# Kernel optimization log

Hardware: AMD Instinct MI355X
Metric: run time of the kernel (lower is better)

Reference implementation:

```python
import jax, jax.numpy as jnp
import numpy as np

DMODEL = 1024
N_EXPERTS = 16
EXPERT_SIZE = 256
K = 4


def setup_inputs() -> dict:
    key = jax.random.key(0)
    k1, k2, k3, k4 = jax.random.split(key, 4)
    std_sel = 1.0 / np.sqrt(DMODEL)
    std_val = 1.0 / np.sqrt(N_EXPERTS * EXPERT_SIZE)
    return {
        "x": jax.random.normal(k1, (4, 2048, DMODEL), dtype=jnp.float32),
        "expert_sel": jax.random.normal(k2, (N_EXPERTS, DMODEL), dtype=jnp.float32) * std_sel,
        "keys": jax.random.normal(k3, (N_EXPERTS, DMODEL, EXPERT_SIZE), dtype=jnp.float32) * std_sel,
        "values": jax.random.normal(k4, (N_EXPERTS, EXPERT_SIZE, DMODEL), dtype=jnp.float32) * std_val,
        "route_scale": jnp.ones((1,), dtype=jnp.float32),
    }


def reference(x, expert_sel, keys, values, route_scale):
    # Routing: sigmoid gating, top-k selection (eval mode: no dropout/bias balancing)
    sel_logits = jnp.einsum("btd,ed->bte", x, expert_sel)  # [B,T,E]
    sel_probs = jax.nn.sigmoid(sel_logits)
    _, sel_index = jax.lax.top_k(sel_probs, K)  # [B,T,K]
    sel_val = jnp.take_along_axis(sel_probs, sel_index, axis=-1)  # [B,T,K]
    sel_val = sel_val / jnp.clip(sel_val.sum(-1, keepdims=True), 1e-9)
    sel_val = sel_val * route_scale  # route_scale shape [1] broadcasts
    # Dense all-expert FFN (as in original), then gather top-k and combine
    scores_all = jax.nn.relu(jnp.einsum("btd,edh->bteh", x, keys))  # [B,T,E,H]
    values_all = jnp.einsum("bteh,ehv->btev", scores_all, values)   # [B,T,E,V]
    sel_idx_exp = sel_index[..., None]  # [B,T,K,1]
    selected = jnp.take_along_axis(values_all, sel_idx_exp, axis=2)  # [B,T,K,V]
    out = (selected * sel_val[..., None]).sum(axis=2)  # [B,T,V]
    return out
```

## Files before the change

### kernel.cpp

```cpp
#include <hip/hip_runtime.h>
#include <math.h>


constexpr int NTOK = 8192;
constexpr int DM   = 1024;
constexpr int NE   = 16;
constexpr int EH   = 256;
constexpr int TK   = 4;
constexpr int CAP  = 8192;
constexpr int TM   = 64;

typedef __attribute__((ext_vector_type(8))) short short8;
typedef __attribute__((ext_vector_type(4))) float f32x4;

#define MFMA16(a, b, c) __builtin_amdgcn_mfma_f32_16x16x32_bf16(a, b, c, 0, 0, 0)

__device__ __forceinline__ void gload_lds16(const void* g, void* l) {
    __builtin_amdgcn_global_load_lds(
        (const __attribute__((address_space(1))) void*)g,
        (__attribute__((address_space(3))) void*)l, 16, 0, 0);
}

__device__ __forceinline__ unsigned short f2bf(float f) {
    union { float f; unsigned int u; } x; x.f = f;
    unsigned int r = x.u + 0x7fffu + ((x.u >> 16) & 1u);
    return (unsigned short)(r >> 16);
}
__device__ __forceinline__ float bf2f(unsigned short b) {
    union { unsigned int u; float f; } x; x.u = ((unsigned int)b) << 16;
    return x.f;
}

__global__ __launch_bounds__(256) void route_conv_kernel(
    const float* __restrict__ x, const float* __restrict__ esel,
    const float* __restrict__ rscale,
    unsigned short* __restrict__ xb,
    int4* __restrict__ sel4, float* __restrict__ wtk)
{
    __shared__ float Es[NE * DM];
    int tid = threadIdx.x;

    {
        const float4* src = (const float4*)esel;
        float4* dst = (float4*)Es;
        #pragma unroll
        for (int j = 0; j < 16; ++j) dst[tid + j * 256] = src[tid + j * 256];
    }
    __syncthreads();

    int t    = blockIdx.x * 8 + (tid >> 5);
    int l32  = tid & 31;

    float acc[NE];
    #pragma unroll
    for (int e = 0; e < NE; ++e) acc[e] = 0.f;

    const float4* x4 = (const float4*)(x + (size_t)t * DM);
    const float4* E4 = (const float4*)Es;
    #pragma unroll
    for (int i4 = 0; i4 < 8; ++i4) {
        int d4 = i4 * 32 + l32;
        float4 xv = x4[d4];
        ushort4 cb = { f2bf(xv.x), f2bf(xv.y), f2bf(xv.z), f2bf(xv.w) };
        *(ushort4*)(xb + (size_t)t * DM + d4 * 4) = cb;
        #pragma unroll
        for (int e = 0; e < NE; ++e) {
            float4 wv = E4[e * 256 + d4];
            acc[e] = fmaf(xv.x, wv.x, acc[e]);
            acc[e] = fmaf(xv.y, wv.y, acc[e]);
            acc[e] = fmaf(xv.z, wv.z, acc[e]);
            acc[e] = fmaf(xv.w, wv.w, acc[e]);
        }
    }

    #pragma unroll
    for (int off = 16; off; off >>= 1)
        #pragma unroll
        for (int e = 0; e < NE; ++e)
            acc[e] += __shfl_xor(acc[e], off, 32);

    if (l32 == 0) {
        float p[NE];
        #pragma unroll
        for (int e = 0; e < NE; ++e) p[e] = 1.0f / (1.0f + expf(-acc[e]));

        int   sel_e[TK];
        float sel_p[TK];
        float sum = 0.f;
        #pragma unroll
        for (int k = 0; k < TK; ++k) {
            float best = -INFINITY; int be = NE;
            #pragma unroll
            for (int e = 0; e < NE; ++e) {
                bool take = p[e] > best;
                best = take ? p[e] : best;
                be   = take ? e    : be;
            }
            sel_e[k] = be; sel_p[k] = best; sum += best;
            #pragma unroll
            for (int e = 0; e < NE; ++e) p[e] = (e == be) ? -INFINITY : p[e];
        }

        float wsc = rscale[0] / fmaxf(sum, 1e-9f);
        int4 s = { sel_e[0], sel_e[1], sel_e[2], sel_e[3] };
        sel4[t] = s;
        float4 wv = { sel_p[0] * wsc, sel_p[1] * wsc,
                      sel_p[2] * wsc, sel_p[3] * wsc };
        *(float4*)(wtk + t * TK) = wv;
    }
}

__global__ __launch_bounds__(1024) void compact_kernel(
    const int4* __restrict__ sel4, int* __restrict__ counts,
    int* __restrict__ lpk)
{
    __shared__ int wsum[16];
    int e    = blockIdx.x;
    int tid  = threadIdx.x;
    int w    = tid >> 6;
    int lane = tid & 63;

    int base = 0;
    for (int c = 0; c < NTOK; c += 1024) {
        int t = c + tid;
        int4 s = sel4[t];
        int k = -1;
        if      (s.x == e) k = 0;
        else if (s.y == e) k = 1;
        else if (s.z == e) k = 2;
        else if (s.w == e) k = 3;
        unsigned long long m = __ballot(k >= 0);
        int rank = __popcll(m & ((1ull << lane) - 1ull));
        if (lane == 63) wsum[w] = __popcll(m);
        __syncthreads();
        int prefix = 0, total = 0;
        #pragma unroll
        for (int i = 0; i < 16; ++i) {
            int v = wsum[i];
            prefix += (i < w) ? v : 0;
            total  += v;
        }
        if (k >= 0) lpk[e * CAP + base + prefix + rank] = t * TK + k;
        base += total;
        __syncthreads();
    }
    if (tid == 0) counts[e] = base;
}

__global__ __launch_bounds__(256) void trans_kernel(
    const float* __restrict__ in, unsigned short* __restrict__ outp, int R, int C)
{
    __shared__ float T[32][33];
    int e = blockIdx.z;
    int r0 = blockIdx.y * 32, c0 = blockIdx.x * 32;
    int ri = threadIdx.x >> 3, cq = threadIdx.x & 7;
    float4 v = *(const float4*)(in + ((size_t)e * R + r0 + ri) * C + c0 + cq * 4);
    T[ri][cq * 4 + 0] = v.x; T[ri][cq * 4 + 1] = v.y;
    T[ri][cq * 4 + 2] = v.z; T[ri][cq * 4 + 3] = v.w;
    __syncthreads();
    int ci = threadIdx.x >> 3, rq = threadIdx.x & 7;
    ushort4 o = { f2bf(T[rq * 4 + 0][ci]), f2bf(T[rq * 4 + 1][ci]),
                  f2bf(T[rq * 4 + 2][ci]), f2bf(T[rq * 4 + 3][ci]) };
    *(ushort4*)(outp + ((size_t)e * C + c0 + ci) * R + r0 + rq * 4) = o;
}

template<int USE_SCRATCH>
__global__ __launch_bounds__(256, 2) void ffn_kernel(
    const unsigned short* __restrict__ xb,
    const unsigned short* __restrict__ ktb,
    const unsigned short* __restrict__ vtb,
    const int* __restrict__ counts, const int* __restrict__ lpk,
    const float* __restrict__ wtk,
    unsigned short* __restrict__ scratch,
    float* __restrict__ out)
{
    int e   = blockIdx.y;
    int cnt = counts[e];
    int t0  = blockIdx.x * TM;
    if (t0 >= cnt) return;

    __shared__ __align__(16) char L[74496];
    char* Xs = L;
    char* KV = L + 8192;
    char* Ss = L + 40960;
    int*   stok = (int*)(L + 73728);
    int*   spk  = (int*)(L + 73984);
    float* sw   = (float*)(L + 74240);

    int tid  = threadIdx.x;
    int lane = tid & 63;
    int w    = tid >> 6;

    if (tid < TM) {
        int s = t0 + tid;
        if (s < cnt) {
            int pk = lpk[e * CAP + s];
            stok[tid] = pk >> 2; spk[tid] = pk; sw[tid] = wtk[pk];
        } else {
            stok[tid] = 0; spk[tid] = USE_SCRATCH ? (NTOK * TK) : 0; sw[tid] = 0.f;
        }
    }
    __syncthreads();

    f32x4 zero = {0.f, 0.f, 0.f, 0.f};
    f32x4 acc[4][4];
    #pragma unroll
    for (int mi = 0; mi < 4; ++mi)
        #pragma unroll
        for (int ni = 0; ni < 4; ++ni) acc[mi][ni] = zero;

    for (int kc = 0; kc < DM; kc += 64) {
        #pragma unroll
        for (int c = 0; c < 2; ++c) {
            int base = (w * 16 + c * 8) * 128;
            int P = base + lane * 16;
            int row = P >> 7;
            int A = P ^ ((row & 7) << 4);
            const unsigned short* src =
                xb + (size_t)stok[A >> 7] * DM + kc + ((A & 127) >> 1);
            gload_lds16(src, Xs + base);
        }
        #pragma unroll
        for (int c = 0; c < 8; ++c) {
            int base = (w * 64 + c * 8) * 128;
            int P = base + lane * 16;
            int row = P >> 7;
            int A = P ^ ((row & 7) << 4);
            const unsigned short* src =
                ktb + ((size_t)e * EH + (A >> 7)) * DM + kc + ((A & 127) >> 1);
            gload_lds16(src, KV + base);
        }
        __syncthreads();
        #pragma unroll
        for (int kk = 0; kk < 2; ++kk) {
            short8 a[4], b[4];
            #pragma unroll
            for (int mi = 0; mi < 4; ++mi) {
                int row = mi * 16 + (lane & 15);
                int A = row * 128 + (kk * 32 + (lane >> 4) * 8) * 2;
                a[mi] = *(const short8*)(Xs + (A ^ ((row & 7) << 4)));
            }
            #pragma unroll
            for (int ni = 0; ni < 4; ++ni) {
                int row = w * 64 + ni * 16 + (lane & 15);
                int A = row * 128 + (kk * 32 + (lane >> 4) * 8) * 2;
                b[ni] = *(const short8*)(KV + (A ^ ((row & 7) << 4)));
            }
            #pragma unroll
            for (int mi = 0; mi < 4; ++mi)
                #pragma unroll
                for (int ni = 0; ni < 4; ++ni)
                    acc[mi][ni] = MFMA16(a[mi], b[ni], acc[mi][ni]);
        }
        __syncthreads();
    }

    #pragma unroll
    for (int mi = 0; mi < 4; ++mi)
        #pragma unroll
        for (int ni = 0; ni < 4; ++ni) {
            f32x4 v = acc[mi][ni];
            #pragma unroll
            for (int r = 0; r < 4; ++r) {
                int row = mi * 16 + (lane >> 4) * 4 + r;
                int col = w * 64 + ni * 16 + (lane & 15);
                int A = row * 512 + col * 2;
                *(unsigned short*)(Ss + (A ^ ((row & 7) << 4))) =
                    f2bf(fmaxf(v[r], 0.f));
            }
        }
    __syncthreads();

    for (int nb = 0; nb < 4; ++nb) {
        f32x4 acc2[4][4];
        #pragma unroll
        for (int mi = 0; mi < 4; ++mi)
            #pragma unroll
            for (int ni = 0; ni < 4; ++ni) acc2[mi][ni] = zero;

        for (int kc = 0; kc < EH; kc += 64) {
            #pragma unroll
            for (int c = 0; c < 8; ++c) {
                int base = (w * 64 + c * 8) * 128;
                int P = base + lane * 16;
                int row = P >> 7;
                int A = P ^ ((row & 7) << 4);
                const unsigned short* src =
                    vtb + ((size_t)e * DM + nb * 256 + (A >> 7)) * EH + kc + ((A & 127) >> 1);
                gload_lds16(src, KV + base);
            }
            __syncthreads();
            #pragma unroll
            for (int kk = 0; kk < 2; ++kk) {
                short8 a[4], b[4];
                #pragma unroll
                for (int mi = 0; mi < 4; ++mi) {
                    int row = mi * 16 + (lane & 15);
                    int A = row * 512 + (kc + kk * 32 + (lane >> 4) * 8) * 2;
                    a[mi] = *(const short8*)(Ss + (A ^ ((row & 7) << 4)));
                }
                #pragma unroll
                for (int ni = 0; ni < 4; ++ni) {
                    int row = w * 64 + ni * 16 + (lane & 15);
                    int A = row * 128 + (kk * 32 + (lane >> 4) * 8) * 2;
                    b[ni] = *(const short8*)(KV + (A ^ ((row & 7) << 4)));
                }
                #pragma unroll
                for (int mi = 0; mi < 4; ++mi)
                    #pragma unroll
                    for (int ni = 0; ni < 4; ++ni)
                        acc2[mi][ni] = MFMA16(a[mi], b[ni], acc2[mi][ni]);
            }
            __syncthreads();
        }

        #pragma unroll
        for (int mi = 0; mi < 4; ++mi)
            #pragma unroll
            for (int ni = 0; ni < 4; ++ni) {
                f32x4 v = acc2[mi][ni];
                #pragma unroll
                for (int r = 0; r < 4; ++r) {
                    int slot = mi * 16 + (lane >> 4) * 4 + r;
                    int d = nb * 256 + w * 64 + ni * 16 + (lane & 15);
                    if (USE_SCRATCH) {
                        scratch[(size_t)spk[slot] * DM + d] = f2bf(v[r]);
                    } else {
                        atomicAdd(out + (size_t)stok[slot] * DM + d, sw[slot] * v[r]);
                    }
                }
            }
    }
}

__global__ __launch_bounds__(256) void combine_kernel(
    const unsigned short* __restrict__ scratch, const float* __restrict__ wtk,
    float* __restrict__ out)
{
    int t  = blockIdx.x * 2 + (threadIdx.x >> 7);
    int d0 = (threadIdx.x & 127) * 8;
    float o[8] = {0.f, 0.f, 0.f, 0.f, 0.f, 0.f, 0.f, 0.f};
    #pragma unroll
    for (int k = 0; k < TK; ++k) {
        float wv = wtk[t * TK + k];
        uint4 q = *(const uint4*)(scratch + (size_t)(t * TK + k) * DM + d0);
        unsigned int us[4] = {q.x, q.y, q.z, q.w};
        #pragma unroll
        for (int j = 0; j < 4; ++j) {
            o[j * 2 + 0] = fmaf(wv, bf2f((unsigned short)(us[j] & 0xffff)), o[j * 2 + 0]);
            o[j * 2 + 1] = fmaf(wv, bf2f((unsigned short)(us[j] >> 16)),    o[j * 2 + 1]);
        }
    }
    float4 w0 = {o[0], o[1], o[2], o[3]}, w1 = {o[4], o[5], o[6], o[7]};
    *(float4*)(out + (size_t)t * DM + d0)     = w0;
    *(float4*)(out + (size_t)t * DM + d0 + 4) = w1;
}

extern "C" void kernel_launch(void* const* d_in, const int* in_sizes, int n_in,
                              void* d_out, int out_size, void* d_ws, size_t ws_size,
                              hipStream_t stream) {
    const float* x      = (const float*)d_in[0];
    const float* esel   = (const float*)d_in[1];
    const float* keys   = (const float*)d_in[2];
    const float* values = (const float*)d_in[3];
    const float* rscale = (const float*)d_in[4];
    float* out = (float*)d_out;

    char* ws = (char*)d_ws;
    size_t o = 0;
    auto alloc = [&](size_t sz) { size_t r = o; o = (o + sz + 255) & ~(size_t)255; return r; };
    size_t o_counts = alloc(NE * 4);
    size_t o_lpk    = alloc((size_t)NE * CAP * 4);
    size_t o_sel4   = alloc((size_t)NTOK * 16);
    size_t o_wtk    = alloc((size_t)NTOK * TK * 4);
    size_t o_xb     = alloc((size_t)NTOK * DM * 2);
    size_t o_ktb    = alloc((size_t)NE * EH * DM * 2);
    size_t o_vtb    = alloc((size_t)NE * DM * EH * 2);
    size_t o_scr    = alloc(((size_t)NTOK * TK + TM) * DM * 2);
    size_t need_full = o;

    int*            counts  = (int*)(ws + o_counts);
    int*            lpk     = (int*)(ws + o_lpk);
    int4*           sel4    = (int4*)(ws + o_sel4);
    float*          wtk     = (float*)(ws + o_wtk);
    unsigned short* xb      = (unsigned short*)(ws + o_xb);
    unsigned short* ktb     = (unsigned short*)(ws + o_ktb);
    unsigned short* vtb     = (unsigned short*)(ws + o_vtb);
    unsigned short* scratch = (unsigned short*)(ws + o_scr);

    bool use_scratch = ws_size >= need_full;

    if (!use_scratch)
        hipMemsetAsync(d_out, 0, (size_t)out_size * sizeof(float), stream);

    route_conv_kernel<<<NTOK / 8, 256, 0, stream>>>(x, esel, rscale, xb,
                                                    sel4, wtk);
    compact_kernel<<<NE, 1024, 0, stream>>>(sel4, counts, lpk);
    trans_kernel<<<dim3(EH / 32, DM / 32, NE), 256, 0, stream>>>(keys, ktb, DM, EH);
    trans_kernel<<<dim3(DM / 32, EH / 32, NE), 256, 0, stream>>>(values, vtb, EH, DM);

    if (use_scratch) {
        ffn_kernel<1><<<dim3(CAP / TM, NE), 256, 0, stream>>>(
            xb, ktb, vtb, counts, lpk, wtk, scratch, out);
        combine_kernel<<<NTOK / 2, 256, 0, stream>>>(scratch, wtk, out);
    } else {
        ffn_kernel<0><<<dim3(CAP / TM, NE), 256, 0, stream>>>(
            xb, ktb, vtb, counts, lpk, wtk, scratch, out);
    }
}
```

Baseline: 147.8 us.

## Load expert weights directly from global memory and remap blocks per XCD

Expert key and value weight tiles are no longer staged in LDS. Each wave now reads its B fragments straight from global memory, relying on L2 and cache reuse across blocks. Blocks are remapped so that each XCD handles two experts, which keeps that expert's weights resident in the local L2. Cutting LDS use to about 41KB and raising launch bounds to 3 blocks per CU aims at higher occupancy and fewer barriers, at the risk of exposed global load latency inside the MFMA loops.

```diff
diff --git a/kernel.cpp b/kernel.cpp
--- a/kernel.cpp
+++ b/kernel.cpp
@@ -165,7 +165,7 @@
 }
 
 template<int USE_SCRATCH>
-__global__ __launch_bounds__(256, 2) void ffn_kernel(
+__global__ __launch_bounds__(256, 3) void ffn_kernel(
     const unsigned short* __restrict__ xb,
     const unsigned short* __restrict__ ktb,
     const unsigned short* __restrict__ vtb,
@@ -174,18 +174,21 @@
     unsigned short* __restrict__ scratch,
     float* __restrict__ out)
 {
-    int e   = blockIdx.y;
+    int flat = blockIdx.y * gridDim.x + blockIdx.x;
+    int xcd  = flat & 7;
+    int ixc  = flat >> 3;
+    int e    = xcd * 2 + (ixc >> 7);
+    int t0   = (ixc & 127) * TM;
+
     int cnt = counts[e];
-    int t0  = blockIdx.x * TM;
     if (t0 >= cnt) return;
 
-    __shared__ __align__(16) char L[74496];
+    __shared__ __align__(16) char L[41728];
     char* Xs = L;
-    char* KV = L + 8192;
-    char* Ss = L + 40960;
-    int*   stok = (int*)(L + 73728);
-    int*   spk  = (int*)(L + 73984);
-    float* sw   = (float*)(L + 74240);
+    char* Ss = L + 8192;
+    int*   stok = (int*)(L + 40960);
+    int*   spk  = (int*)(L + 41216);
+    float* sw   = (float*)(L + 41472);
 
     int tid  = threadIdx.x;
     int lane = tid & 63;
@@ -209,6 +212,7 @@
         #pragma unroll
         for (int ni = 0; ni < 4; ++ni) acc[mi][ni] = zero;
 
+    const unsigned short* kbase = ktb + (size_t)e * EH * DM;
     for (int kc = 0; kc < DM; kc += 64) {
         #pragma unroll
         for (int c = 0; c < 2; ++c) {
@@ -220,16 +224,6 @@
                 xb + (size_t)stok[A >> 7] * DM + kc + ((A & 127) >> 1);
             gload_lds16(src, Xs + base);
         }
-        #pragma unroll
-        for (int c = 0; c < 8; ++c) {
-            int base = (w * 64 + c * 8) * 128;
-            int P = base + lane * 16;
-            int row = P >> 7;
-            int A = P ^ ((row & 7) << 4);
-            const unsigned short* src =
-                ktb + ((size_t)e * EH + (A >> 7)) * DM + kc + ((A & 127) >> 1);
-            gload_lds16(src, KV + base);
-        }
         __syncthreads();
         #pragma unroll
         for (int kk = 0; kk < 2; ++kk) {
@@ -242,9 +236,9 @@
             }
             #pragma unroll
             for (int ni = 0; ni < 4; ++ni) {
-                int row = w * 64 + ni * 16 + (lane & 15);
-                int A = row * 128 + (kk * 32 + (lane >> 4) * 8) * 2;
-                b[ni] = *(const short8*)(KV + (A ^ ((row & 7) << 4)));
+                int h = w * 64 + ni * 16 + (lane & 15);
+                b[ni] = *(const short8*)(kbase + (size_t)h * DM + kc +
+                                         kk * 32 + (lane >> 4) * 8);
             }
             #pragma unroll
             for (int mi = 0; mi < 4; ++mi)
@@ -271,47 +265,34 @@
         }
     __syncthreads();
 
-    for (int nb = 0; nb < 4; ++nb) {
+    const unsigned short* vbase = vtb + (size_t)e * DM * EH;
+    for (int nc = 0; nc < 4; ++nc) {
         f32x4 acc2[4][4];
         #pragma unroll
         for (int mi = 0; mi < 4; ++mi)
             #pragma unroll
             for (int ni = 0; ni < 4; ++ni) acc2[mi][ni] = zero;
 
-        for (int kc = 0; kc < EH; kc += 64) {
-            #pragma unroll
-            for (int c = 0; c < 8; ++c) {
-                int base = (w * 64 + c * 8) * 128;
-                int P = base + lane * 16;
-                int row = P >> 7;
-                int A = P ^ ((row & 7) << 4);
-                const unsigned short* src =
-                    vtb + ((size_t)e * DM + nb * 256 + (A >> 7)) * EH + kc + ((A & 127) >> 1);
-                gload_lds16(src, KV + base);
-            }
-            __syncthreads();
-            #pragma unroll
-            for (int kk = 0; kk < 2; ++kk) {
-                short8 a[4], b[4];
+        #pragma unroll
+        for (int kk = 0; kk < 8; ++kk) {
+            short8 a[4], b[4];
+            #pragma unroll
+            for (int mi = 0; mi < 4; ++mi) {
+                int row = mi * 16 + (lane & 15);
+                int A = row * 512 + (kk * 32 + (lane >> 4) * 8) * 2;
+                a[mi] = *(const short8*)(Ss + (A ^ ((row & 7) << 4)));
+            }
+            #pragma unroll
+            for (int ni = 0; ni < 4; ++ni) {
+                int d = w * 256 + nc * 64 + ni * 16 + (lane & 15);
+                b[ni] = *(const short8*)(vbase + (size_t)d * EH +
+                                         kk * 32 + (lane >> 4) * 8);
+            }
+            #pragma unroll
+            for (int mi = 0; mi < 4; ++mi)
                 #pragma unroll
-                for (int mi = 0; mi < 4; ++mi) {
-                    int row = mi * 16 + (lane & 15);
-                    int A = row * 512 + (kc + kk * 32 + (lane >> 4) * 8) * 2;
-                    a[mi] = *(const short8*)(Ss + (A ^ ((row & 7) << 4)));
-                }
-                #pragma unroll
-                for (int ni = 0; ni < 4; ++ni) {
-                    int row = w * 64 + ni * 16 + (lane & 15);
-                    int A = row * 128 + (kk * 32 + (lane >> 4) * 8) * 2;
-                    b[ni] = *(const short8*)(KV + (A ^ ((row & 7) << 4)));
-                }
-                #pragma unroll
-                for (int mi = 0; mi < 4; ++mi)
-                    #pragma unroll
-                    for (int ni = 0; ni < 4; ++ni)
-                        acc2[mi][ni] = MFMA16(a[mi], b[ni], acc2[mi][ni]);
-            }
-            __syncthreads();
+                for (int ni = 0; ni < 4; ++ni)
+                    acc2[mi][ni] = MFMA16(a[mi], b[ni], acc2[mi][ni]);
         }
 
         #pragma unroll
@@ -322,7 +303,7 @@
                 #pragma unroll
                 for (int r = 0; r < 4; ++r) {
                     int slot = mi * 16 + (lane >> 4) * 4 + r;
-                    int d = nb * 256 + w * 64 + ni * 16 + (lane & 15);
+                    int d = w * 256 + nc * 64 + ni * 16 + (lane & 15);
                     if (USE_SCRATCH) {
                         scratch[(size_t)spk[slot] * DM + d] = f2bf(v[r]);
                     } else {
```

New measurement: 206.4 us. +39.6%, slower.
